# Performance work log

Measured on AMD Instinct MI355X. Metric: run time of the kernel, lower is better.

Reference implementation:

```python
import jax, jax.numpy as jnp
import numpy as np

CONF_THRES = 0.25
IOU_THRES = 0.45
MAX_DET = 300      # max detections returned (padded/masked to static shape)
K = 8192           # top-K score candidates entering NMS (static bound)
N_ANCHORS = 102000 # YOLOv5 @ 1280px
NC = 80            # COCO classes


def setup_inputs() -> dict:
    key = jax.random.key(0)
    # [B=1, N, 4 (xywh) + 1 (obj) + 80 (cls)] raw head predictions in [0,1)
    preds = jax.random.uniform(key, (1, N_ANCHORS, 4 + 1 + NC), dtype=jnp.float32)
    return {"preds": preds}


def _xywh2yxyx(b):
    # (xc, yc, w, h) -> (y1, x1, y2, x2), matching pt_xywh2yxyx_yolo
    x, y, w, h = b[..., 0], b[..., 1], b[..., 2], b[..., 3]
    return jnp.stack([y - h * 0.5, x - w * 0.5, y + h * 0.5, x + w * 0.5], axis=-1)


def _iou_matrix(boxes):
    # boxes: [K, 4] in yxyx; returns pairwise IoU [K, K]
    area = (boxes[:, 2] - boxes[:, 0]) * (boxes[:, 3] - boxes[:, 1])
    ty = jnp.maximum(boxes[:, None, 0], boxes[None, :, 0])
    tx = jnp.maximum(boxes[:, None, 1], boxes[None, :, 1])
    by = jnp.minimum(boxes[:, None, 2], boxes[None, :, 2])
    bx = jnp.minimum(boxes[:, None, 3], boxes[None, :, 3])
    inter = jnp.clip(by - ty, 0.0) * jnp.clip(bx - tx, 0.0)
    union = area[:, None] + area[None, :] - inter
    return inter / (union + 1e-9)


def _yolo_nms(preds):
    p = preds[0]                       # [N, 85] (loop returns on first image)
    obj = p[:, 4]                      # objectness
    cand = obj > CONF_THRES            # confidence filter
    cls_scores = p[:, 5:] * obj[:, None]
    scores = jnp.max(cls_scores, axis=1)
    classes = jnp.argmax(cls_scores, axis=1).astype(jnp.float32)
    scores = jnp.where(cand, scores, 0.0)  # mask instead of dynamic filter
    boxes = _xywh2yxyx(p[:, :4])       # [N, 4] yxyx

    # top-K candidates by score (static replacement for boolean filtering)
    top_scores, idx = jax.lax.top_k(scores, K)
    top_boxes = boxes[idx]
    top_classes = classes[idx]
    valid = top_scores > 0.0

    iou = _iou_matrix(top_boxes)       # [K, K], 256 MB fp32

    # greedy NMS: boxes already sorted by descending score
    ar = jnp.arange(K)

    def body(i, suppressed):
        keep_i = jnp.logical_and(jnp.logical_not(suppressed[i]), valid[i])
        return suppressed | (keep_i & (iou[i] > IOU_THRES) & (ar > i))

    suppressed = jax.lax.fori_loop(0, K, body, jnp.zeros((K,), jnp.bool_))
    keep = valid & jnp.logical_not(suppressed)

    # gather top MAX_DET kept detections (sorted), zero-pad the rest
    keep_scores = jnp.where(keep, top_scores, -1.0)
    _, sel = jax.lax.top_k(keep_scores, MAX_DET)
    mask = keep[sel]
    out_boxes = jnp.where(mask[:, None], top_boxes[sel], 0.0)[None]    # [1, MAX_DET, 4]
    out_classes = jnp.where(mask, top_classes[sel], 0.0)[None]         # [1, MAX_DET]
    out_scores = jnp.where(mask, top_scores[sel], 0.0)[None]           # [1, MAX_DET]
    return out_boxes, out_classes, out_scores


def reference(preds):
    return _yolo_nms(preds)
```

## Files before the change

### kernel.cpp

```cpp
#include <hip/hip_runtime.h>
#include <cstdint>

#define CONF_THRES 0.25f
#define IOU_THRES  0.45f
#define MAX_DET    300
#define K_TOP      8192
#define NA         102000
#define NCLS       80
#define ROWLEN     85
#define CAP        32640
#define NPLANE     8
#define NBINS      16384
#define WIN        512
#define NWIN       (K_TOP / WIN)
#define SSTR       9

typedef unsigned long long u64;
typedef unsigned int u32;

__global__ __launch_bounds__(256) void zero_kernel(uint4* __restrict__ a,
        uint4* __restrict__ r, uint4* __restrict__ b) {
    int i = blockIdx.x * 256 + threadIdx.x;
    uint4 z = make_uint4(0u, 0u, 0u, 0u);
    if (i < 4164) a[i] = z;
    if (i < 8160) r[i] = z;
    b[i] = z;
}

__global__ __launch_bounds__(256) void score_key_kernel(const float* __restrict__ preds,
        u64* __restrict__ keys, u32* __restrict__ histP) {
#pragma clang fp contract(off)
    int lane = threadIdx.x & 63;
    int i = blockIdx.x * 4 + (threadIdx.x >> 6);
    if (i >= NA) return;
    const float* p = preds + (size_t)i * ROWLEN;
    float v0 = p[lane];
    float v1 = (lane < ROWLEN - 64) ? p[64 + lane] : 0.0f;
    float obj = __shfl(v0, 4);
    float m = (lane >= 5) ? v0 : 0.0f;
    m = fmaxf(m, (lane < 21) ? v1 : 0.0f);
    for (int off = 32; off; off >>= 1) m = fmaxf(m, __shfl_xor(m, off));
    if (lane == 0) {
        float score = (obj > CONF_THRES) ? m * obj : 0.0f;
        u32 sb = __float_as_uint(score);
        keys[i] = ((u64)sb << 32) | (u32)(~(u32)i);
        if (sb != 0u)
            atomicAdd(&histP[((u32)blockIdx.x & (NPLANE - 1u)) * NBINS + (sb >> 16)], 1u);
    }
}

__global__ __launch_bounds__(256) void reduce_hist_kernel(const u32* __restrict__ histP,
        u32* __restrict__ sumhist) {
    int bin = blockIdx.x * 256 + threadIdx.x;
    u32 s = 0;
#pragma unroll
    for (int r = 0; r < NPLANE; ++r) s += histP[r * NBINS + bin];
    sumhist[bin] = s;
}

__global__ __launch_bounds__(1024) void cutoff_kernel(const u32* __restrict__ hist,
        u32* __restrict__ meta) {
    __shared__ u32 suf[1024];
    __shared__ int cbs;
    __shared__ u32 above_s;
    int t = threadIdx.x;
    u32 s = 0;
    const u32* hb = hist + t * 16;
    for (int b = 0; b < 16; ++b) s += hb[b];
    suf[t] = s;
    if (t == 0) { cbs = -1; above_s = 0; }
    __syncthreads();
    for (int off = 1; off < 1024; off <<= 1) {
        u32 add = (t + off < 1024) ? suf[t + off] : 0u;
        __syncthreads();
        suf[t] += add;
        __syncthreads();
    }
    u32 st = suf[t];
    u32 stn = (t < 1023) ? suf[t + 1] : 0u;
    if (st >= (u32)K_TOP && stn < (u32)K_TOP) {
        cbs = t;
        above_s = stn;
    }
    __syncthreads();
    int cb = cbs;
    if (t < 64) {
        u32 thresh = 0;
        if (cb >= 0) {
            u32 above = above_s;
            u32 v = (t < 16) ? hist[cb * 16 + t] : 0u;
            for (int off = 1; off < 64; off <<= 1) {
                u32 o = __shfl_down(v, off);
                if (t + off < 64) v += o;
            }
            u64 bal = __ballot(v + above >= (u32)K_TOP);
            int bstar = 63 - __builtin_clzll((unsigned long long)bal);
            thresh = ((u32)(cb * 16 + bstar)) << 16;
        }
        if (t == 0) meta[1] = thresh;
    }
}

__global__ __launch_bounds__(256) void compact_kernel(const u64* __restrict__ keys,
        u32* __restrict__ meta, u64* __restrict__ comp) {
    __shared__ u32 woff[4];
    __shared__ u32 bbase;
    int i = blockIdx.x * 256 + threadIdx.x;
    int wid = threadIdx.x >> 6, lane = threadIdx.x & 63;
    u64 key = (i < NA) ? keys[i] : 0ull;
    u32 sb = (u32)(key >> 32);
    u32 th = meta[1];
    bool take = (i < NA) && (sb != 0u) && (sb >= th);
    u64 bal = __ballot(take);
    if (lane == 0) woff[wid] = (u32)__popcll(bal);
    __syncthreads();
    if (threadIdx.x == 0) {
        u32 t0 = woff[0], t1 = woff[1], t2 = woff[2], t3 = woff[3];
        bbase = atomicAdd(&meta[0], t0 + t1 + t2 + t3);
        woff[0] = 0; woff[1] = t0; woff[2] = t0 + t1; woff[3] = t0 + t1 + t2;
    }
    __syncthreads();
    if (take) {
        u32 pos = bbase + woff[wid] + (u32)__popcll(bal & ((1ull << lane) - 1ull));
        if (pos < CAP) comp[pos] = key;
    }
}

__global__ __launch_bounds__(256) void rank_partial_kernel(const u64* __restrict__ comp,
        const u32* __restrict__ meta, u32* __restrict__ rankArr) {
    __shared__ u64 tile[1024];
    u32 cnt = meta[0];
    int n = (int)(cnt < (u32)CAP ? cnt : (u32)CAP);
    int i0 = blockIdx.x * 256;
    int j0 = blockIdx.y * 1024;
    if (i0 >= n || j0 >= n) return;
    int lim = n - j0; if (lim > 1024) lim = 1024;
    for (int k = threadIdx.x; k < 1024; k += 256)
        tile[k] = (k < lim) ? comp[j0 + k] : 0ull;
    __syncthreads();
    int i = i0 + threadIdx.x;
    if (i < n) {
        u64 key = comp[i];
        u32 r = 0;
#pragma unroll 8
        for (int j = 0; j < 1024; ++j) r += (tile[j] > key) ? 1u : 0u;
        atomicAdd(&rankArr[i], r);
    }
}

__global__ __launch_bounds__(256) void scatter_kernel(const u64* __restrict__ comp,
        const u32* __restrict__ meta, const u32* __restrict__ rankArr,
        u64* __restrict__ sorted) {
    u32 cnt = meta[0];
    int n = (int)(cnt < (u32)CAP ? cnt : (u32)CAP);
    int i = blockIdx.x * 256 + threadIdx.x;
    if (i < n) {
        u32 r = rankArr[i];
        if (r < (u32)K_TOP) sorted[r] = comp[i];
    }
}

__global__ __launch_bounds__(256) void gather_kernel(const u64* __restrict__ sorted,
        const float* __restrict__ preds, float* __restrict__ boxes,
        float* __restrict__ scores, float* __restrict__ classes,
        float* __restrict__ areas) {
#pragma clang fp contract(off)
    int lane = threadIdx.x & 63;
    int i = blockIdx.x * 4 + (threadIdx.x >> 6);
    u64 key = sorted[i];
    u32 sb = (u32)(key >> 32);
    float score = __uint_as_float(sb);
    if (score > 0.0f) {
        u32 idx = ~(u32)(key & 0xffffffffull);
        const float* p = preds + (size_t)idx * ROWLEN;
        float v0 = p[lane];
        float v1 = (lane < ROWLEN - 64) ? p[64 + lane] : 0.0f;
        float obj = __shfl(v0, 4);
        u64 kb = 0;
        if (lane >= 5) {
            float q = v0 * obj;
            kb = ((u64)__float_as_uint(q) << 8) | (u32)(255 - (lane - 5));
        }
        if (lane < 21) {
            float q = v1 * obj;
            u64 kb2 = ((u64)__float_as_uint(q) << 8) | (u32)(255 - (59 + lane));
            if (kb2 > kb) kb = kb2;
        }
        for (int off = 32; off; off >>= 1) {
            u64 o = __shfl_xor(kb, off);
            if (o > kb) kb = o;
        }
        u32 cls = 255u - (u32)(kb & 0xffull);
        float x = __shfl(v0, 0), y = __shfl(v0, 1);
        float w = __shfl(v0, 2), h = __shfl(v0, 3);
        if (lane == 0) {
            float ymin = y - h * 0.5f, xmin = x - w * 0.5f;
            float ymax = y + h * 0.5f, xmax = x + w * 0.5f;
            boxes[i * 4 + 0] = ymin;
            boxes[i * 4 + 1] = xmin;
            boxes[i * 4 + 2] = ymax;
            boxes[i * 4 + 3] = xmax;
            scores[i] = score;
            classes[i] = (float)cls;
            areas[i] = (ymax - ymin) * (xmax - xmin);
        }
    } else if (lane == 0) {
        boxes[i * 4 + 0] = 0.0f; boxes[i * 4 + 1] = 0.0f;
        boxes[i * 4 + 2] = 0.0f; boxes[i * 4 + 3] = 0.0f;
        scores[i] = 0.0f;
        classes[i] = 0.0f;
        areas[i] = 0.0f;
    }
}

__global__ __launch_bounds__(256) void mask_kernel(const float* __restrict__ boxes,
        const float* __restrict__ areas, const float* __restrict__ scores,
        u64* __restrict__ mask, u64* __restrict__ remw) {
#pragma clang fp contract(off)
    int cx = blockIdx.x;
    int ry = blockIdx.y;
    if (cx < (ry >> 2)) return;
    __shared__ float4 cb[256];
    __shared__ float  ca[256];
    __shared__ u64 st[64 * 5];
    int tid = threadIdx.x;
    int wv = tid >> 6, lane = tid & 63;
    int r0 = ry * 64;
    int jw = cx * 4 + wv;
    cb[tid] = ((const float4*)boxes)[cx * 256 + tid];
    ca[tid] = areas[cx * 256 + tid];
    if (cx == (ry >> 2) && wv == 0) {
        u64 b = __ballot(scores[r0 + lane] > 0.0f);
        if (lane == 0) remw[ry] = b;
    }
    __syncthreads();
    u64 myword = 0;
    if (jw >= ry) {
        float4 bi = ((const float4*)boxes)[r0 + lane];
        float ai = areas[r0 + lane];
        const double Bd = (double)IOU_THRES + 0x1p-26;
        int kb = wv * 64;
#pragma unroll
        for (int k = 0; k < 64; ++k) {
            float4 bj = cb[kb + k];
            float aj = ca[kb + k];
            float ty = fmaxf(bi.x, bj.x);
            float tx = fmaxf(bi.y, bj.y);
            float by = fminf(bi.z, bj.z);
            float bx = fminf(bi.w, bj.w);
            float inter = fmaxf(by - ty, 0.0f) * fmaxf(bx - tx, 0.0f);
            float uni = (ai + aj) - inter;
            float u = uni + 1e-9f;
            bool sup = ((double)inter > Bd * (double)u);
            myword |= sup ? (1ull << k) : 0ull;
        }
        if (jw == ry)
            myword &= (lane < 63) ? (~0ull << (lane + 1)) : 0ull;
    }
    st[lane * 5 + wv] = myword;
    __syncthreads();
    mask[(size_t)(r0 + (tid >> 2)) * 128 + cx * 4 + (tid & 3)] =
            st[(tid >> 2) * 5 + (tid & 3)];
}

__device__ __forceinline__ u64 rfl64(u64 v) {
    u32 lo = (u32)__builtin_amdgcn_readfirstlane((int)(u32)v);
    u32 hi = (u32)__builtin_amdgcn_readfirstlane((int)(u32)(v >> 32));
    return ((u64)hi << 32) | lo;
}

__device__ __forceinline__ u64 bcast64(u64 v, int srclane) {
    u32 lo = (u32)__builtin_amdgcn_readlane((int)(u32)v, srclane);
    u32 hi = (u32)__builtin_amdgcn_readlane((int)(u32)(v >> 32), srclane);
    return ((u64)hi << 32) | lo;
}

__device__ __forceinline__ u64 shfl_xor64(u64 v, int m) {
    u32 lo = __shfl_xor((u32)v, m, 64);
    u32 hi = __shfl_xor((u32)(v >> 32), m, 64);
    return ((u64)hi << 32) | lo;
}

__global__ __launch_bounds__(256) void nms_scan_kernel(const u64* __restrict__ mask,
        const u64* __restrict__ remw, const float* __restrict__ boxes,
        const float* __restrict__ scores, const float* __restrict__ classes,
        float* __restrict__ out) {
    __shared__ u64 sub[2][WIN * SSTR];
    __shared__ u64 accW[4][8];
    __shared__ u32 ki[MAX_DET + 8];
    __shared__ int n_sh;
    int tid = threadIdx.x;
    int wid = tid >> 6, lane = tid & 63;
    if (tid == 0) n_sh = 0;
#pragma unroll
    for (int it = 0; it < 8; ++it) {
        int idx = it * 256 + tid;
        int r = idx >> 2, j = (idx & 3) * 2;
        uint4 v = *(const uint4*)&mask[(size_t)r * 128 + j];
        sub[0][r * SSTR + j]     = ((u64)v.y << 32) | v.x;
        sub[0][r * SSTR + j + 1] = ((u64)v.w << 32) | v.z;
    }
    __syncthreads();
    int n = 0;
    for (int win = 0; win < NWIN; ++win) {
        if (n >= MAX_DET) break;
        int rbase = win * WIN;
        int cb = win & 1;
        u64 acc[8] = {0, 0, 0, 0, 0, 0, 0, 0};
        for (int m = tid; m < n; m += 256) {
            int k = (int)ki[m];
            const u64* rp = &mask[(size_t)k * 128 + win * 8];
#pragma unroll
            for (int j = 0; j < 8; ++j) acc[j] |= rp[j];
        }
#pragma unroll
        for (int j = 0; j < 8; ++j)
            for (int off = 32; off; off >>= 1) acc[j] |= shfl_xor64(acc[j], off);
        if (lane == 0) {
#pragma unroll
            for (int j = 0; j < 8; ++j) accW[wid][j] = acc[j];
        }
        __syncthreads();
        if (wid != 0) {
            if (win + 1 < NWIN) {
                int t = tid - 64;
                for (int it = 0; it < 11; ++it) {
                    int idx = it * 192 + t;
                    if (idx < 2048) {
                        int r = idx >> 2, j = (idx & 3) * 2;
                        uint4 v = *(const uint4*)&mask[
                                (size_t)(rbase + WIN + r) * 128 + (win + 1) * 8 + j];
                        sub[cb ^ 1][r * SSTR + j]     = ((u64)v.y << 32) | v.x;
                        sub[cb ^ 1][r * SSTR + j + 1] = ((u64)v.w << 32) | v.z;
                    }
                }
            }
        } else {
            u64 diag[8];
#pragma unroll
            for (int sw = 0; sw < 8; ++sw)
                diag[sw] = sub[cb][(sw * 64 + lane) * SSTR + sw];
            int n0 = n;
            u64 keptW[8] = {0, 0, 0, 0, 0, 0, 0, 0};
#pragma unroll
            for (int sw = 0; sw < 8; ++sw) {
                if (n < MAX_DET) {
                    u64 acc2 = 0;
#pragma unroll
                    for (int wp = 0; wp < 8; ++wp) {
                        if (wp < sw) {
                            if ((keptW[wp] >> lane) & 1ull)
                                acc2 |= sub[cb][(wp * 64 + lane) * SSTR + sw];
                        }
                    }
                    for (int off = 32; off; off >>= 1) acc2 |= shfl_xor64(acc2, off);
                    u64 afold = accW[0][sw] | accW[1][sw] | accW[2][sw] | accW[3][sw];
                    u64 cur = rfl64(remw[win * 8 + sw]) & ~rfl64(afold) & ~rfl64(acc2);
                    u64 kw = 0;
                    while (cur != 0ull && n < MAX_DET) {
                        int b = __ffsll((unsigned long long)cur) - 1;
                        u64 slice = bcast64(diag[sw], b);
                        kw |= (1ull << b);
                        cur &= ~(slice | (1ull << b));
                        ++n;
                    }
                    keptW[sw] = kw;
                }
            }
            int base = n0;
#pragma unroll
            for (int sw = 0; sw < 8; ++sw) {
                u64 kw = keptW[sw];
                if ((kw >> lane) & 1ull) {
                    int rr = (int)__popcll(kw & ((1ull << lane) - 1ull));
                    ki[base + rr] = (u32)(rbase + sw * 64 + lane);
                }
                base += (int)__popcll(kw);
            }
            if (lane == 0) n_sh = n;
        }
        __syncthreads();
        n = n_sh;
    }
    __syncthreads();
    for (int m = tid; m < MAX_DET; m += 256) {
        float4 b = make_float4(0.0f, 0.0f, 0.0f, 0.0f);
        float c = 0.0f, s = 0.0f;
        if (m < n) {
            int k = (int)ki[m];
            b = ((const float4*)boxes)[k];
            c = classes[k];
            s = scores[k];
        }
        ((float4*)out)[m] = b;
        out[1200 + m] = c;
        out[1500 + m] = s;
    }
}

extern "C" void kernel_launch(void* const* d_in, const int* in_sizes, int n_in,
                              void* d_out, int out_size, void* d_ws, size_t ws_size,
                              hipStream_t stream) {
    const float* preds = (const float*)d_in[0];
    char* ws = (char*)d_ws;

    u32*   sumhist = (u32*)(ws + 0);
    u32*   rankArr = (u32*)(ws + 65536);
    u32*   meta    = (u32*)(ws + 262144);
    u64*   remw    = (u64*)(ws + 262208);
    u64*   sorted  = (u64*)(ws + 263232);
    u64*   keys    = (u64*)(ws + 328768);
    u64*   comp    = (u64*)(ws + 1144768);
    float* careas  = (float*)(ws + 1144768);
    float* tboxes  = (float*)(ws + 1405888);
    float* tscores = (float*)(ws + 1536960);
    float* tclass  = (float*)(ws + 1569728);
    u64*   mask    = (u64*)(ws + 1602496);
    u32*   histP   = (u32*)(ws + 1602496);
    float* out     = (float*)d_out;

    zero_kernel<<<128, 256, 0, stream>>>((uint4*)(ws + 262144), (uint4*)rankArr,
            (uint4*)histP);
    score_key_kernel<<<(NA + 3) / 4, 256, 0, stream>>>(preds, keys, histP);
    reduce_hist_kernel<<<64, 256, 0, stream>>>(histP, sumhist);
    cutoff_kernel<<<1, 1024, 0, stream>>>(sumhist, meta);
    compact_kernel<<<(NA + 255) / 256, 256, 0, stream>>>(keys, meta, comp);
    rank_partial_kernel<<<dim3((CAP + 255) / 256, (CAP + 1023) / 1024), 256, 0, stream>>>(
            comp, meta, rankArr);
    scatter_kernel<<<(CAP + 255) / 256, 256, 0, stream>>>(comp, meta, rankArr, sorted);
    gather_kernel<<<K_TOP / 4, 256, 0, stream>>>(sorted, preds, tboxes, tscores,
            tclass, careas);
    mask_kernel<<<dim3(32, 128), 256, 0, stream>>>(tboxes, careas, tscores, mask, remw);
    nms_scan_kernel<<<1, 256, 0, stream>>>(mask, remw, tboxes, tscores, tclass, out);
}
```

Before: 193.3 us.

## Precompute box records in scoring pass and process two row-words per mask block

The scoring kernel now computes the argmax class, converted box and area for every anchor and writes them as a compact 32-byte record. The gather kernel reads that record with one thread per candidate instead of re-reading the 85-float prediction row with a full wavefront. The histogram reduction kernel is removed: the cutoff kernel sums the planes directly, and there are now 4 planes instead of 8. The mask kernel handles 128 rows per block, halving the grid and reusing the shared-memory column tile. The cost is an extra ~3 MB of record writes for all anchors in the scoring pass, plus more contention on the atomic histogram.

```diff
diff --git a/kernel.cpp b/kernel.cpp
--- a/kernel.cpp
+++ b/kernel.cpp
@@ -9,7 +9,7 @@
 #define NCLS       80
 #define ROWLEN     85
 #define CAP        32640
-#define NPLANE     8
+#define NPLANE     4
 #define NBINS      16384
 #define WIN        512
 #define NWIN       (K_TOP / WIN)
@@ -28,7 +28,7 @@
 }
 
 __global__ __launch_bounds__(256) void score_key_kernel(const float* __restrict__ preds,
-        u64* __restrict__ keys, u32* __restrict__ histP) {
+        u64* __restrict__ keys, u32* __restrict__ histP, float4* __restrict__ recs) {
 #pragma clang fp contract(off)
     int lane = threadIdx.x & 63;
     int i = blockIdx.x * 4 + (threadIdx.x >> 6);
@@ -37,36 +37,49 @@
     float v0 = p[lane];
     float v1 = (lane < ROWLEN - 64) ? p[64 + lane] : 0.0f;
     float obj = __shfl(v0, 4);
-    float m = (lane >= 5) ? v0 : 0.0f;
-    m = fmaxf(m, (lane < 21) ? v1 : 0.0f);
-    for (int off = 32; off; off >>= 1) m = fmaxf(m, __shfl_xor(m, off));
+    u64 kb = 0;
+    if (lane >= 5) {
+        float q = v0 * obj;
+        kb = ((u64)__float_as_uint(q) << 8) | (u32)(255 - (lane - 5));
+    }
+    if (lane < 21) {
+        float q = v1 * obj;
+        u64 kb2 = ((u64)__float_as_uint(q) << 8) | (u32)(255 - (59 + lane));
+        if (kb2 > kb) kb = kb2;
+    }
+    for (int off = 32; off; off >>= 1) {
+        u64 o = __shfl_xor(kb, off);
+        if (o > kb) kb = o;
+    }
+    float x = __shfl(v0, 0), y = __shfl(v0, 1);
+    float w = __shfl(v0, 2), h = __shfl(v0, 3);
     if (lane == 0) {
-        float score = (obj > CONF_THRES) ? m * obj : 0.0f;
+        float maxq = __uint_as_float((u32)(kb >> 8));
+        float score = (obj > CONF_THRES) ? maxq : 0.0f;
         u32 sb = __float_as_uint(score);
+        u32 cls = 255u - (u32)(kb & 0xffull);
+        float ymin = y - h * 0.5f, xmin = x - w * 0.5f;
+        float ymax = y + h * 0.5f, xmax = x + w * 0.5f;
         keys[i] = ((u64)sb << 32) | (u32)(~(u32)i);
+        recs[2 * i]     = make_float4(ymin, xmin, ymax, xmax);
+        recs[2 * i + 1] = make_float4(score, (float)cls,
+                                      (ymax - ymin) * (xmax - xmin), 0.0f);
         if (sb != 0u)
             atomicAdd(&histP[((u32)blockIdx.x & (NPLANE - 1u)) * NBINS + (sb >> 16)], 1u);
     }
 }
 
-__global__ __launch_bounds__(256) void reduce_hist_kernel(const u32* __restrict__ histP,
-        u32* __restrict__ sumhist) {
-    int bin = blockIdx.x * 256 + threadIdx.x;
-    u32 s = 0;
-#pragma unroll
-    for (int r = 0; r < NPLANE; ++r) s += histP[r * NBINS + bin];
-    sumhist[bin] = s;
-}
-
-__global__ __launch_bounds__(1024) void cutoff_kernel(const u32* __restrict__ hist,
+__global__ __launch_bounds__(1024) void cutoff_kernel(const u32* __restrict__ histP,
         u32* __restrict__ meta) {
     __shared__ u32 suf[1024];
     __shared__ int cbs;
     __shared__ u32 above_s;
     int t = threadIdx.x;
     u32 s = 0;
-    const u32* hb = hist + t * 16;
-    for (int b = 0; b < 16; ++b) s += hb[b];
+    for (int r = 0; r < NPLANE; ++r) {
+        const u32* hb = histP + r * NBINS + t * 16;
+        for (int b = 0; b < 16; ++b) s += hb[b];
+    }
     suf[t] = s;
     if (t == 0) { cbs = -1; above_s = 0; }
     __syncthreads();
@@ -88,7 +101,10 @@
         u32 thresh = 0;
         if (cb >= 0) {
             u32 above = above_s;
-            u32 v = (t < 16) ? hist[cb * 16 + t] : 0u;
+            u32 v = 0;
+            if (t < 16) {
+                for (int r = 0; r < NPLANE; ++r) v += histP[r * NBINS + cb * 16 + t];
+            }
             for (int off = 1; off < 64; off <<= 1) {
                 u32 o = __shfl_down(v, off);
                 if (t + off < 64) v += o;
@@ -161,56 +177,25 @@
 }
 
 __global__ __launch_bounds__(256) void gather_kernel(const u64* __restrict__ sorted,
-        const float* __restrict__ preds, float* __restrict__ boxes,
+        const float4* __restrict__ recs, float* __restrict__ boxes,
         float* __restrict__ scores, float* __restrict__ classes,
         float* __restrict__ areas) {
-#pragma clang fp contract(off)
-    int lane = threadIdx.x & 63;
-    int i = blockIdx.x * 4 + (threadIdx.x >> 6);
+    int i = blockIdx.x * 256 + threadIdx.x;
     u64 key = sorted[i];
     u32 sb = (u32)(key >> 32);
     float score = __uint_as_float(sb);
+    float4 b = make_float4(0.0f, 0.0f, 0.0f, 0.0f);
+    float c = 0.0f, a = 0.0f;
     if (score > 0.0f) {
         u32 idx = ~(u32)(key & 0xffffffffull);
-        const float* p = preds + (size_t)idx * ROWLEN;
-        float v0 = p[lane];
-        float v1 = (lane < ROWLEN - 64) ? p[64 + lane] : 0.0f;
-        float obj = __shfl(v0, 4);
-        u64 kb = 0;
-        if (lane >= 5) {
-            float q = v0 * obj;
-            kb = ((u64)__float_as_uint(q) << 8) | (u32)(255 - (lane - 5));
-        }
-        if (lane < 21) {
-            float q = v1 * obj;
-            u64 kb2 = ((u64)__float_as_uint(q) << 8) | (u32)(255 - (59 + lane));
-            if (kb2 > kb) kb = kb2;
-        }
-        for (int off = 32; off; off >>= 1) {
-            u64 o = __shfl_xor(kb, off);
-            if (o > kb) kb = o;
-        }
-        u32 cls = 255u - (u32)(kb & 0xffull);
-        float x = __shfl(v0, 0), y = __shfl(v0, 1);
-        float w = __shfl(v0, 2), h = __shfl(v0, 3);
-        if (lane == 0) {
-            float ymin = y - h * 0.5f, xmin = x - w * 0.5f;
-            float ymax = y + h * 0.5f, xmax = x + w * 0.5f;
-            boxes[i * 4 + 0] = ymin;
-            boxes[i * 4 + 1] = xmin;
-            boxes[i * 4 + 2] = ymax;
-            boxes[i * 4 + 3] = xmax;
-            scores[i] = score;
-            classes[i] = (float)cls;
-            areas[i] = (ymax - ymin) * (xmax - xmin);
-        }
-    } else if (lane == 0) {
-        boxes[i * 4 + 0] = 0.0f; boxes[i * 4 + 1] = 0.0f;
-        boxes[i * 4 + 2] = 0.0f; boxes[i * 4 + 3] = 0.0f;
-        scores[i] = 0.0f;
-        classes[i] = 0.0f;
-        areas[i] = 0.0f;
-    }
+        float4 r0 = recs[2 * idx];
+        float4 r1 = recs[2 * idx + 1];
+        b = r0; c = r1.y; a = r1.z;
+    }
+    ((float4*)boxes)[i] = b;
+    scores[i] = score;
+    classes[i] = c;
+    areas[i] = a;
 }
 
 __global__ __launch_bounds__(256) void mask_kernel(const float* __restrict__ boxes,
@@ -219,48 +204,70 @@
 #pragma clang fp contract(off)
     int cx = blockIdx.x;
     int ry = blockIdx.y;
-    if (cx < (ry >> 2)) return;
+    int wr0 = ry * 2;
+    if (cx * 4 + 3 < wr0) return;
     __shared__ float4 cb[256];
     __shared__ float  ca[256];
-    __shared__ u64 st[64 * 5];
+    __shared__ u64 st[128 * 5];
     int tid = threadIdx.x;
     int wv = tid >> 6, lane = tid & 63;
-    int r0 = ry * 64;
+    int r0 = ry * 128;
     int jw = cx * 4 + wv;
     cb[tid] = ((const float4*)boxes)[cx * 256 + tid];
     ca[tid] = areas[cx * 256 + tid];
-    if (cx == (ry >> 2) && wv == 0) {
+    if (jw == wr0) {
         u64 b = __ballot(scores[r0 + lane] > 0.0f);
-        if (lane == 0) remw[ry] = b;
-    }
-    __syncthreads();
-    u64 myword = 0;
-    if (jw >= ry) {
-        float4 bi = ((const float4*)boxes)[r0 + lane];
-        float ai = areas[r0 + lane];
+        if (lane == 0) remw[wr0] = b;
+    }
+    if (jw == wr0 + 1) {
+        u64 b = __ballot(scores[r0 + 64 + lane] > 0.0f);
+        if (lane == 0) remw[wr0 + 1] = b;
+    }
+    __syncthreads();
+    u64 wA = 0, wB = 0;
+    if (jw >= wr0) {
+        float4 biA = ((const float4*)boxes)[r0 + lane];
+        float aiA = areas[r0 + lane];
+        float4 biB = ((const float4*)boxes)[r0 + 64 + lane];
+        float aiB = areas[r0 + 64 + lane];
         const double Bd = (double)IOU_THRES + 0x1p-26;
         int kb = wv * 64;
 #pragma unroll
         for (int k = 0; k < 64; ++k) {
             float4 bj = cb[kb + k];
             float aj = ca[kb + k];
-            float ty = fmaxf(bi.x, bj.x);
-            float tx = fmaxf(bi.y, bj.y);
-            float by = fminf(bi.z, bj.z);
-            float bx = fminf(bi.w, bj.w);
-            float inter = fmaxf(by - ty, 0.0f) * fmaxf(bx - tx, 0.0f);
-            float uni = (ai + aj) - inter;
-            float u = uni + 1e-9f;
-            bool sup = ((double)inter > Bd * (double)u);
-            myword |= sup ? (1ull << k) : 0ull;
-        }
-        if (jw == ry)
-            myword &= (lane < 63) ? (~0ull << (lane + 1)) : 0ull;
-    }
-    st[lane * 5 + wv] = myword;
-    __syncthreads();
-    mask[(size_t)(r0 + (tid >> 2)) * 128 + cx * 4 + (tid & 3)] =
-            st[(tid >> 2) * 5 + (tid & 3)];
+            float tyA = fmaxf(biA.x, bj.x);
+            float txA = fmaxf(biA.y, bj.y);
+            float byA = fminf(biA.z, bj.z);
+            float bxA = fminf(biA.w, bj.w);
+            float inA = fmaxf(byA - tyA, 0.0f) * fmaxf(bxA - txA, 0.0f);
+            float uA = ((aiA + aj) - inA) + 1e-9f;
+            wA |= ((double)inA > Bd * (double)uA) ? (1ull << k) : 0ull;
+            float tyB = fmaxf(biB.x, bj.x);
+            float txB = fmaxf(biB.y, bj.y);
+            float byB = fminf(biB.z, bj.z);
+            float bxB = fminf(biB.w, bj.w);
+            float inB = fmaxf(byB - tyB, 0.0f) * fmaxf(bxB - txB, 0.0f);
+            float uB = ((aiB + aj) - inB) + 1e-9f;
+            wB |= ((double)inB > Bd * (double)uB) ? (1ull << k) : 0ull;
+        }
+        if (jw == wr0)
+            wA &= (lane < 63) ? (~0ull << (lane + 1)) : 0ull;
+        if (jw < wr0 + 1) {
+            if (jw == wr0) wB = 0;
+        }
+        if (jw == wr0 + 1)
+            wB &= (lane < 63) ? (~0ull << (lane + 1)) : 0ull;
+    }
+    st[lane * 5 + wv] = wA;
+    st[(lane + 64) * 5 + wv] = wB;
+    __syncthreads();
+#pragma unroll
+    for (int q = 0; q < 2; ++q) {
+        int idx = q * 256 + tid;
+        int rr = idx >> 2, ww = idx & 3;
+        mask[(size_t)(r0 + rr) * 128 + cx * 4 + ww] = st[rr * 5 + ww];
+    }
 }
 
 __device__ __forceinline__ u64 rfl64(u64 v) {
@@ -404,32 +411,31 @@
     const float* preds = (const float*)d_in[0];
     char* ws = (char*)d_ws;
 
-    u32*   sumhist = (u32*)(ws + 0);
     u32*   rankArr = (u32*)(ws + 65536);
     u32*   meta    = (u32*)(ws + 262144);
     u64*   remw    = (u64*)(ws + 262208);
     u64*   sorted  = (u64*)(ws + 263232);
     u64*   keys    = (u64*)(ws + 328768);
     u64*   comp    = (u64*)(ws + 1144768);
-    float* careas  = (float*)(ws + 1144768);
+    float* tareas  = (float*)(ws + 1144768);
     float* tboxes  = (float*)(ws + 1405888);
     float* tscores = (float*)(ws + 1536960);
     float* tclass  = (float*)(ws + 1569728);
     u64*   mask    = (u64*)(ws + 1602496);
     u32*   histP   = (u32*)(ws + 1602496);
+    float4* recs   = (float4*)(ws + 2126784);
     float* out     = (float*)d_out;
 
-    zero_kernel<<<128, 256, 0, stream>>>((uint4*)(ws + 262144), (uint4*)rankArr,
+    zero_kernel<<<64, 256, 0, stream>>>((uint4*)(ws + 262144), (uint4*)rankArr,
             (uint4*)histP);
-    score_key_kernel<<<(NA + 3) / 4, 256, 0, stream>>>(preds, keys, histP);
-    reduce_hist_kernel<<<64, 256, 0, stream>>>(histP, sumhist);
-    cutoff_kernel<<<1, 1024, 0, stream>>>(sumhist, meta);
+    score_key_kernel<<<(NA + 3) / 4, 256, 0, stream>>>(preds, keys, histP, recs);
+    cutoff_kernel<<<1, 1024, 0, stream>>>(histP, meta);
     compact_kernel<<<(NA + 255) / 256, 256, 0, stream>>>(keys, meta, comp);
     rank_partial_kernel<<<dim3((CAP + 255) / 256, (CAP + 1023) / 1024), 256, 0, stream>>>(
             comp, meta, rankArr);
     scatter_kernel<<<(CAP + 255) / 256, 256, 0, stream>>>(comp, meta, rankArr, sorted);
-    gather_kernel<<<K_TOP / 4, 256, 0, stream>>>(sorted, preds, tboxes, tscores,
-            tclass, careas);
-    mask_kernel<<<dim3(32, 128), 256, 0, stream>>>(tboxes, careas, tscores, mask, remw);
+    gather_kernel<<<K_TOP / 256, 256, 0, stream>>>(sorted, recs, tboxes, tscores,
+            tclass, tareas);
+    mask_kernel<<<dim3(32, 64), 256, 0, stream>>>(tboxes, tareas, tscores, mask, remw);
     nms_scan_kernel<<<1, 256, 0, stream>>>(mask, remw, tboxes, tscores, tclass, out);
 }
```

Result: slower. 203.3 us (+5.2%).
